# Optimization experiments

Measured on AMD Instinct MI355X. Metric: run time of the kernel, lower is better.

## Reference

```python
import jax, jax.numpy as jnp
import numpy as np

NUM_EXPERTS = 64
TOP_K = 8
N_GROUP = 8
TOPK_GROUP = 4
HIDDEN = 1024
INTER = 512
TOKENS = 2048


def setup_inputs() -> dict:
    key = jax.random.key(0)
    k1, k2, k3, k4 = jax.random.split(key, 4)
    return {
        "hidden_states": jax.random.normal(k1, (TOKENS, HIDDEN), jnp.float32),
        "gate_w": jax.random.normal(k2, (NUM_EXPERTS, HIDDEN), jnp.float32) * 0.02,
        "e_score_correction_bias": jnp.zeros((NUM_EXPERTS,), jnp.float32),
        "w13": jax.random.normal(k3, (NUM_EXPERTS, 2 * INTER, HIDDEN), jnp.float32) * 0.02,
        "w2": jax.random.normal(k4, (NUM_EXPERTS, HIDDEN, INTER), jnp.float32) * 0.02,
    }


def _grouped_topk(scores, bias):
    # DeepSeek-V3 style grouped top-k with sigmoid scores + correction bias.
    T, E = scores.shape
    s = scores + bias[None, :]                            # [T, E] selection scores
    sg = s.reshape(T, N_GROUP, E // N_GROUP)              # [T, G, E/G]
    top2 = jax.lax.top_k(sg, 2)[0]                        # [T, G, 2]
    group_scores = top2.sum(-1)                           # [T, G]
    _, gidx = jax.lax.top_k(group_scores, TOPK_GROUP)     # [T, topk_group]
    gmask = jnp.zeros((T, N_GROUP), bool).at[jnp.arange(T)[:, None], gidx].set(True)
    emask = jnp.repeat(gmask, E // N_GROUP, axis=1)       # [T, E]
    masked = jnp.where(emask, s, -jnp.inf)
    _, topk_ids = jax.lax.top_k(masked, TOP_K)            # [T, K]
    topk_w = jnp.take_along_axis(scores, topk_ids, axis=1)  # weights use raw scores (no bias)
    topk_w = topk_w / jnp.sum(topk_w, axis=-1, keepdims=True)  # renormalize (norm_topk_prob)
    return topk_w, topk_ids


def reference(hidden_states, gate_w, e_score_correction_bias, w13, w2):
    x = hidden_states                                      # [T, H]
    T, H = x.shape
    router_logits = x.astype(jnp.float32) @ gate_w.T       # fp32 gate, [T, E]
    scores = jax.nn.sigmoid(router_logits)
    topk_w, topk_ids = _grouped_topk(scores, e_score_correction_bias)
    # dense token->expert routing weights [T, E]
    R = jnp.zeros((T, NUM_EXPERTS), x.dtype).at[
        jnp.arange(T)[:, None], topk_ids
    ].add(topk_w.astype(x.dtype))

    def body(acc, inp):
        w13_e, w2_e, r_e = inp
        gu = x @ w13_e.T                                   # [T, 2I]
        g, u = jnp.split(gu, 2, axis=-1)
        h = jax.nn.silu(g) * u                             # SwiGLU
        return acc + r_e[:, None] * (h @ w2_e.T), None

    y, _ = jax.lax.scan(body, jnp.zeros_like(x), (w13, w2, R.T))
    return y
```

## Files before the change

### kernel.cpp

```cpp
#include <hip/hip_runtime.h>
#include <hip/hip_bf16.h>

#define TOKENS 2048
#define HDIM 1024
#define IDIM 512
#define NEXP 64
#define TOPKK 8
#define NGRP 8
#define TOPG 4

typedef __bf16 bf16_t;
typedef __bf16 bf16x8 __attribute__((ext_vector_type(8)));
typedef __bf16 bf16x4 __attribute__((ext_vector_type(4)));
typedef float f32x4 __attribute__((ext_vector_type(4)));

#define SWZ(r, b) ((b) ^ (((r) & 7) << 4))

__device__ inline bf16x8 pack_bf16x8(float4 a, float4 b) {
  bf16x8 r;
  r[0] = (bf16_t)a.x; r[1] = (bf16_t)a.y; r[2] = (bf16_t)a.z; r[3] = (bf16_t)a.w;
  r[4] = (bf16_t)b.x; r[5] = (bf16_t)b.y; r[6] = (bf16_t)b.z; r[7] = (bf16_t)b.w;
  return r;
}

__global__ __launch_bounds__(256) void cvt_x_kernel(const float* __restrict__ x,
                                                    bf16_t* __restrict__ xb) {
  int i = blockIdx.x * 256 + threadIdx.x;
  float4 v = reinterpret_cast<const float4*>(x)[i];
  bf16x4 o;
  o[0] = (bf16_t)v.x; o[1] = (bf16_t)v.y; o[2] = (bf16_t)v.z; o[3] = (bf16_t)v.w;
  reinterpret_cast<bf16x4*>(xb)[i] = o;
}

__global__ __launch_bounds__(256) void router_kernel(
    const float* __restrict__ x, const float* __restrict__ gw,
    const float* __restrict__ bias, int* __restrict__ counts,
    int* __restrict__ tok_list, int* __restrict__ dst_list,
    float* __restrict__ wgt_list) {
  int t0 = blockIdx.x * 16;
  int tid = threadIdx.x;
  int e = tid & 63;
  int sub = tid >> 6;

  const float4* gwe = reinterpret_cast<const float4*>(gw + (size_t)e * HDIM);
  const float4* x0 = reinterpret_cast<const float4*>(x + (size_t)(t0 + sub * 4 + 0) * HDIM);
  const float4* x1 = reinterpret_cast<const float4*>(x + (size_t)(t0 + sub * 4 + 1) * HDIM);
  const float4* x2 = reinterpret_cast<const float4*>(x + (size_t)(t0 + sub * 4 + 2) * HDIM);
  const float4* x3 = reinterpret_cast<const float4*>(x + (size_t)(t0 + sub * 4 + 3) * HDIM);
  float a0 = 0.f, a1 = 0.f, a2 = 0.f, a3 = 0.f;
  for (int h = 0; h < HDIM / 4; ++h) {
    float4 g = gwe[h];
    float4 v;
    v = x0[h]; a0 += g.x * v.x + g.y * v.y + g.z * v.z + g.w * v.w;
    v = x1[h]; a1 += g.x * v.x + g.y * v.y + g.z * v.z + g.w * v.w;
    v = x2[h]; a2 += g.x * v.x + g.y * v.y + g.z * v.z + g.w * v.w;
    v = x3[h]; a3 += g.x * v.x + g.y * v.y + g.z * v.z + g.w * v.w;
  }
  __shared__ float sc[16][64];
  sc[sub * 4 + 0][e] = a0;
  sc[sub * 4 + 1][e] = a1;
  sc[sub * 4 + 2][e] = a2;
  sc[sub * 4 + 3][e] = a3;
  __syncthreads();

  int lane = tid & 63;
  int wv = tid >> 6;
  for (int it = 0; it < 4; ++it) {
    int tt = wv * 4 + it;
    int t = t0 + tt;
    float logit = sc[tt][lane];
    float score = 1.0f / (1.0f + __expf(-logit));
    float s = score + bias[lane];

    float m1 = s, m2 = -INFINITY;
#pragma unroll
    for (int off = 1; off < 8; off <<= 1) {
      float o1 = __shfl_xor(m1, off);
      float o2 = __shfl_xor(m2, off);
      float hi = fmaxf(m1, o1);
      float lo = fminf(m1, o1);
      m2 = fmaxf(lo, fmaxf(m2, o2));
      m1 = hi;
    }
    float gscore = m1 + m2;
    int g = lane >> 3;
    int grank = 0;
#pragma unroll
    for (int gg = 0; gg < 8; ++gg) {
      float og = __shfl(gscore, gg << 3);
      grank += ((og > gscore) || (og == gscore && gg < g)) ? 1 : 0;
    }
    float masked = (grank < TOPG) ? s : -INFINITY;

    int rank = 0;
    for (int l = 0; l < 64; ++l) {
      float ov = __shfl(masked, l);
      rank += ((ov > masked) || (ov == masked && l < lane)) ? 1 : 0;
    }
    bool sel = (rank < TOPKK) && (masked > -INFINITY);
    float part = sel ? score : 0.0f;
#pragma unroll
    for (int off = 32; off > 0; off >>= 1) part += __shfl_xor(part, off);
    if (sel) {
      int slot = atomicAdd(&counts[lane], 1);
      tok_list[lane * TOKENS + slot] = t;
      dst_list[lane * TOKENS + slot] = t * TOPKK + rank;
      wgt_list[lane * TOKENS + slot] = score / part;
    }
  }
}

__global__ __launch_bounds__(256, 2) void gemm1_kernel(
    const bf16_t* __restrict__ xb, const float* __restrict__ w13,
    const int* __restrict__ counts, const int* __restrict__ tok_list,
    const int* __restrict__ dst_list, bf16_t* __restrict__ hbuf) {
  int e = blockIdx.z;
  int cnt = counts[e];
  int row0 = blockIdx.y * 256;
  if (row0 >= cnt) return;
  int rows = cnt - row0;
  if (rows > 256) rows = 256;
  int n0 = blockIdx.x * 64;

  __shared__ alignas(16) char As[256 * 128];
  __shared__ alignas(16) char Bg[64 * 128];
  __shared__ alignas(16) char Bu[64 * 128];
  __shared__ int dstS[256];

  int tid = threadIdx.x;
  int tok = -1;
  if (tid < rows) {
    tok = tok_list[e * TOKENS + row0 + tid];
    dstS[tid] = dst_list[e * TOKENS + row0 + tid];
  }
  const bf16_t* xrow = (tok >= 0) ? (xb + (size_t)tok * HDIM) : (const bf16_t*)0;

  int lane = tid & 63;
  int wv = tid >> 6;

  f32x4 accg[4][4], accu[4][4];
#pragma unroll
  for (int i = 0; i < 4; ++i)
#pragma unroll
    for (int j = 0; j < 4; ++j) {
      accg[i][j] = f32x4{0.f, 0.f, 0.f, 0.f};
      accu[i][j] = f32x4{0.f, 0.f, 0.f, 0.f};
    }

  const float* w13e = w13 + (size_t)e * (2 * IDIM) * HDIM;
  int bn = tid >> 2;
  int bq = tid & 3;
  const float* gsrc = w13e + (size_t)(n0 + bn) * HDIM + bq * 16;
  const float* usrc = w13e + (size_t)(IDIM + n0 + bn) * HDIM + bq * 16;

  for (int kt = 0; kt < 16; ++kt) {
    __syncthreads();
    if (tid < rows) {
      const bf16_t* src = xrow + kt * 64;
#pragma unroll
      for (int j = 0; j < 8; ++j) {
        bf16x8 v = *reinterpret_cast<const bf16x8*>(src + j * 8);
        *reinterpret_cast<bf16x8*>(&As[SWZ(tid, tid * 128 + j * 16)]) = v;
      }
    }
    {
      const float4* s4 = reinterpret_cast<const float4*>(gsrc + kt * 64);
      float4 f0 = s4[0], f1 = s4[1], f2 = s4[2], f3 = s4[3];
      int b0 = bn * 128 + bq * 32;
      *reinterpret_cast<bf16x8*>(&Bg[SWZ(bn, b0)]) = pack_bf16x8(f0, f1);
      *reinterpret_cast<bf16x8*>(&Bg[SWZ(bn, b0 + 16)]) = pack_bf16x8(f2, f3);
      const float4* u4 = reinterpret_cast<const float4*>(usrc + kt * 64);
      f0 = u4[0]; f1 = u4[1]; f2 = u4[2]; f3 = u4[3];
      *reinterpret_cast<bf16x8*>(&Bu[SWZ(bn, b0)]) = pack_bf16x8(f0, f1);
      *reinterpret_cast<bf16x8*>(&Bu[SWZ(bn, b0 + 16)]) = pack_bf16x8(f2, f3);
    }
    __syncthreads();
#pragma unroll
    for (int ks = 0; ks < 2; ++ks) {
      int kb2 = (ks * 32 + ((lane >> 4) << 3)) * 2;
      bf16x8 a[4], bg[4], bu[4];
#pragma unroll
      for (int i = 0; i < 4; ++i) {
        int r = wv * 64 + i * 16 + (lane & 15);
        a[i] = *reinterpret_cast<const bf16x8*>(&As[SWZ(r, r * 128 + kb2)]);
      }
#pragma unroll
      for (int j = 0; j < 4; ++j) {
        int n = j * 16 + (lane & 15);
        bg[j] = *reinterpret_cast<const bf16x8*>(&Bg[SWZ(n, n * 128 + kb2)]);
        bu[j] = *reinterpret_cast<const bf16x8*>(&Bu[SWZ(n, n * 128 + kb2)]);
      }
#pragma unroll
      for (int i = 0; i < 4; ++i)
#pragma unroll
        for (int j = 0; j < 4; ++j) {
          accg[i][j] = __builtin_amdgcn_mfma_f32_16x16x32_bf16(a[i], bg[j], accg[i][j], 0, 0, 0);
          accu[i][j] = __builtin_amdgcn_mfma_f32_16x16x32_bf16(a[i], bu[j], accu[i][j], 0, 0, 0);
        }
    }
  }
#pragma unroll
  for (int i = 0; i < 4; ++i) {
    int mbase = wv * 64 + i * 16 + ((lane >> 4) << 2);
#pragma unroll
    for (int r = 0; r < 4; ++r) {
      int m = mbase + r;
      if (m < rows) {
        int dst = dstS[m];
        bf16_t* hrow = hbuf + (size_t)dst * IDIM + n0;
#pragma unroll
        for (int j = 0; j < 4; ++j) {
          float gv = accg[i][j][r];
          float uv = accu[i][j][r];
          float hv = (gv / (1.0f + __expf(-gv))) * uv;
          hrow[j * 16 + (lane & 15)] = (bf16_t)hv;
        }
      }
    }
  }
}

__global__ __launch_bounds__(256, 2) void gemm2_kernel(
    const bf16_t* __restrict__ hbuf, const float* __restrict__ w2,
    const int* __restrict__ counts, const int* __restrict__ tok_list,
    const int* __restrict__ dst_list, const float* __restrict__ wgt_list,
    float* __restrict__ y) {
  int e = blockIdx.z;
  int cnt = counts[e];
  int row0 = blockIdx.y * 256;
  if (row0 >= cnt) return;
  int rows = cnt - row0;
  if (rows > 256) rows = 256;
  int n0 = blockIdx.x * 64;

  __shared__ alignas(16) char As[256 * 128];
  __shared__ alignas(16) char Bs[64 * 128];
  __shared__ int tokS[256];
  __shared__ float wS[256];

  int tid = threadIdx.x;
  int dst = -1;
  if (tid < rows) {
    tokS[tid] = tok_list[e * TOKENS + row0 + tid];
    dst = dst_list[e * TOKENS + row0 + tid];
    wS[tid] = wgt_list[e * TOKENS + row0 + tid];
  }
  const bf16_t* hrow = (dst >= 0) ? (hbuf + (size_t)dst * IDIM) : (const bf16_t*)0;

  int lane = tid & 63;
  int wv = tid >> 6;
  f32x4 acc[4][4];
#pragma unroll
  for (int i = 0; i < 4; ++i)
#pragma unroll
    for (int j = 0; j < 4; ++j) acc[i][j] = f32x4{0.f, 0.f, 0.f, 0.f};

  const float* w2e = w2 + (size_t)e * HDIM * IDIM;
  int bn = tid >> 2;
  int bq = tid & 3;
  const float* bsrc = w2e + (size_t)(n0 + bn) * IDIM + bq * 16;

  for (int kt = 0; kt < 8; ++kt) {
    __syncthreads();
    if (tid < rows) {
      const bf16_t* src = hrow + kt * 64;
#pragma unroll
      for (int j = 0; j < 8; ++j) {
        bf16x8 v = *reinterpret_cast<const bf16x8*>(src + j * 8);
        *reinterpret_cast<bf16x8*>(&As[SWZ(tid, tid * 128 + j * 16)]) = v;
      }
    }
    {
      const float4* s4 = reinterpret_cast<const float4*>(bsrc + kt * 64);
      float4 f0 = s4[0], f1 = s4[1], f2 = s4[2], f3 = s4[3];
      int b0 = bn * 128 + bq * 32;
      *reinterpret_cast<bf16x8*>(&Bs[SWZ(bn, b0)]) = pack_bf16x8(f0, f1);
      *reinterpret_cast<bf16x8*>(&Bs[SWZ(bn, b0 + 16)]) = pack_bf16x8(f2, f3);
    }
    __syncthreads();
#pragma unroll
    for (int ks = 0; ks < 2; ++ks) {
      int kb2 = (ks * 32 + ((lane >> 4) << 3)) * 2;
      bf16x8 a[4], b[4];
#pragma unroll
      for (int i = 0; i < 4; ++i) {
        int r = wv * 64 + i * 16 + (lane & 15);
        a[i] = *reinterpret_cast<const bf16x8*>(&As[SWZ(r, r * 128 + kb2)]);
      }
#pragma unroll
      for (int j = 0; j < 4; ++j) {
        int n = j * 16 + (lane & 15);
        b[j] = *reinterpret_cast<const bf16x8*>(&Bs[SWZ(n, n * 128 + kb2)]);
      }
#pragma unroll
      for (int i = 0; i < 4; ++i)
#pragma unroll
        for (int j = 0; j < 4; ++j)
          acc[i][j] = __builtin_amdgcn_mfma_f32_16x16x32_bf16(a[i], b[j], acc[i][j], 0, 0, 0);
    }
  }
#pragma unroll
  for (int i = 0; i < 4; ++i) {
    int mbase = wv * 64 + i * 16 + ((lane >> 4) << 2);
#pragma unroll
    for (int r = 0; r < 4; ++r) {
      int m = mbase + r;
      if (m < rows) {
        float wgt = wS[m];
        float* yrow = y + (size_t)tokS[m] * HDIM + n0;
#pragma unroll
        for (int j = 0; j < 4; ++j) {
          atomicAdd(&yrow[j * 16 + (lane & 15)], acc[i][j][r] * wgt);
        }
      }
    }
  }
}

extern "C" void kernel_launch(void* const* d_in, const int* in_sizes, int n_in,
                              void* d_out, int out_size, void* d_ws, size_t ws_size,
                              hipStream_t stream) {
  const float* x = (const float*)d_in[0];
  const float* gw = (const float*)d_in[1];
  const float* bias = (const float*)d_in[2];
  const float* w13 = (const float*)d_in[3];
  const float* w2 = (const float*)d_in[4];
  float* y = (float*)d_out;

  char* ws = (char*)d_ws;
  const size_t LIST = (size_t)NEXP * TOKENS * 4;
  int* counts = (int*)ws;
  int* tok_list = (int*)(ws + 1024);
  int* dst_list = (int*)(ws + 1024 + LIST);
  float* wgt_list = (float*)(ws + 1024 + 2 * LIST);
  bf16_t* xb = (bf16_t*)(ws + 1024 + 3 * LIST);
  bf16_t* hbuf = (bf16_t*)(ws + 1024 + 3 * LIST + (size_t)TOKENS * HDIM * 2);

  hipMemsetAsync(counts, 0, 1024, stream);
  hipMemsetAsync(y, 0, (size_t)TOKENS * HDIM * sizeof(float), stream);
  cvt_x_kernel<<<dim3(TOKENS * HDIM / 4 / 256), 256, 0, stream>>>(x, xb);
  router_kernel<<<dim3(TOKENS / 16), 256, 0, stream>>>(x, gw, bias, counts, tok_list,
                                                       dst_list, wgt_list);
  gemm1_kernel<<<dim3(IDIM / 64, 8, NEXP), 256, 0, stream>>>(xb, w13, counts, tok_list,
                                                             dst_list, hbuf);
  gemm2_kernel<<<dim3(HDIM / 64, 8, NEXP), 256, 0, stream>>>(hbuf, w2, counts, tok_list,
                                                             dst_list, wgt_list, y);
}
```

Before: 890.9 us.

## Prefetch next K-tile into registers during MFMA in both expert GEMM kernels

Both the gate/up and down-projection kernels now load the next K-slice of activations and fp32 weights into registers before running the MFMAs on the current slice, then write it to shared memory after a barrier. This register double-buffering is meant to hide global-memory latency behind the matrix math. A sched_barrier keeps the compiler from sinking the loads past the MFMAs. It costs extra registers, which can lower occupancy.

New measurement: 890.2 us. Within noise of the previous version (-0.1%).

```diff
diff --git a/kernel.cpp b/kernel.cpp
--- a/kernel.cpp
+++ b/kernel.cpp
@@ -152,29 +152,46 @@
   int bq = tid & 3;
   const float* gsrc = w13e + (size_t)(n0 + bn) * HDIM + bq * 16;
   const float* usrc = w13e + (size_t)(IDIM + n0 + bn) * HDIM + bq * 16;
+  int b0 = bn * 128 + bq * 32;
+
+  bf16x8 ra[8];
+  float4 rg[4], ru[4];
+
+  if (tid < rows) {
+#pragma unroll
+    for (int j = 0; j < 8; ++j) ra[j] = *reinterpret_cast<const bf16x8*>(xrow + j * 8);
+  }
+  {
+    const float4* g4 = reinterpret_cast<const float4*>(gsrc);
+    const float4* u4 = reinterpret_cast<const float4*>(usrc);
+#pragma unroll
+    for (int j = 0; j < 4; ++j) { rg[j] = g4[j]; ru[j] = u4[j]; }
+  }
+  if (tid < rows) {
+#pragma unroll
+    for (int j = 0; j < 8; ++j)
+      *reinterpret_cast<bf16x8*>(&As[SWZ(tid, tid * 128 + j * 16)]) = ra[j];
+  }
+  *reinterpret_cast<bf16x8*>(&Bg[SWZ(bn, b0)]) = pack_bf16x8(rg[0], rg[1]);
+  *reinterpret_cast<bf16x8*>(&Bg[SWZ(bn, b0 + 16)]) = pack_bf16x8(rg[2], rg[3]);
+  *reinterpret_cast<bf16x8*>(&Bu[SWZ(bn, b0)]) = pack_bf16x8(ru[0], ru[1]);
+  *reinterpret_cast<bf16x8*>(&Bu[SWZ(bn, b0 + 16)]) = pack_bf16x8(ru[2], ru[3]);
+  __syncthreads();
 
   for (int kt = 0; kt < 16; ++kt) {
-    __syncthreads();
-    if (tid < rows) {
-      const bf16_t* src = xrow + kt * 64;
-#pragma unroll
-      for (int j = 0; j < 8; ++j) {
-        bf16x8 v = *reinterpret_cast<const bf16x8*>(src + j * 8);
-        *reinterpret_cast<bf16x8*>(&As[SWZ(tid, tid * 128 + j * 16)]) = v;
-      }
-    }
-    {
-      const float4* s4 = reinterpret_cast<const float4*>(gsrc + kt * 64);
-      float4 f0 = s4[0], f1 = s4[1], f2 = s4[2], f3 = s4[3];
-      int b0 = bn * 128 + bq * 32;
-      *reinterpret_cast<bf16x8*>(&Bg[SWZ(bn, b0)]) = pack_bf16x8(f0, f1);
-      *reinterpret_cast<bf16x8*>(&Bg[SWZ(bn, b0 + 16)]) = pack_bf16x8(f2, f3);
-      const float4* u4 = reinterpret_cast<const float4*>(usrc + kt * 64);
-      f0 = u4[0]; f1 = u4[1]; f2 = u4[2]; f3 = u4[3];
-      *reinterpret_cast<bf16x8*>(&Bu[SWZ(bn, b0)]) = pack_bf16x8(f0, f1);
-      *reinterpret_cast<bf16x8*>(&Bu[SWZ(bn, b0 + 16)]) = pack_bf16x8(f2, f3);
-    }
-    __syncthreads();
+    if (kt < 15) {
+      if (tid < rows) {
+        const bf16_t* s = xrow + (kt + 1) * 64;
+#pragma unroll
+        for (int j = 0; j < 8; ++j) ra[j] = *reinterpret_cast<const bf16x8*>(s + j * 8);
+      }
+      const float4* g4 = reinterpret_cast<const float4*>(gsrc + (kt + 1) * 64);
+      const float4* u4 = reinterpret_cast<const float4*>(usrc + (kt + 1) * 64);
+#pragma unroll
+      for (int j = 0; j < 4; ++j) { rg[j] = g4[j]; ru[j] = u4[j]; }
+    }
+    __builtin_amdgcn_sched_barrier(0);
+
 #pragma unroll
     for (int ks = 0; ks < 2; ++ks) {
       int kb2 = (ks * 32 + ((lane >> 4) << 3)) * 2;
@@ -197,6 +214,19 @@
           accg[i][j] = __builtin_amdgcn_mfma_f32_16x16x32_bf16(a[i], bg[j], accg[i][j], 0, 0, 0);
           accu[i][j] = __builtin_amdgcn_mfma_f32_16x16x32_bf16(a[i], bu[j], accu[i][j], 0, 0, 0);
         }
+    }
+    __syncthreads();
+    if (kt < 15) {
+      if (tid < rows) {
+#pragma unroll
+        for (int j = 0; j < 8; ++j)
+          *reinterpret_cast<bf16x8*>(&As[SWZ(tid, tid * 128 + j * 16)]) = ra[j];
+      }
+      *reinterpret_cast<bf16x8*>(&Bg[SWZ(bn, b0)]) = pack_bf16x8(rg[0], rg[1]);
+      *reinterpret_cast<bf16x8*>(&Bg[SWZ(bn, b0 + 16)]) = pack_bf16x8(rg[2], rg[3]);
+      *reinterpret_cast<bf16x8*>(&Bu[SWZ(bn, b0)]) = pack_bf16x8(ru[0], ru[1]);
+      *reinterpret_cast<bf16x8*>(&Bu[SWZ(bn, b0 + 16)]) = pack_bf16x8(ru[2], ru[3]);
+      __syncthreads();
     }
   }
 #pragma unroll
@@ -259,25 +289,42 @@
   int bn = tid >> 2;
   int bq = tid & 3;
   const float* bsrc = w2e + (size_t)(n0 + bn) * IDIM + bq * 16;
+  int b0 = bn * 128 + bq * 32;
+
+  bf16x8 rh[8];
+  float4 rb[4];
+
+  if (tid < rows) {
+#pragma unroll
+    for (int j = 0; j < 8; ++j) rh[j] = *reinterpret_cast<const bf16x8*>(hrow + j * 8);
+  }
+  {
+    const float4* s4 = reinterpret_cast<const float4*>(bsrc);
+#pragma unroll
+    for (int j = 0; j < 4; ++j) rb[j] = s4[j];
+  }
+  if (tid < rows) {
+#pragma unroll
+    for (int j = 0; j < 8; ++j)
+      *reinterpret_cast<bf16x8*>(&As[SWZ(tid, tid * 128 + j * 16)]) = rh[j];
+  }
+  *reinterpret_cast<bf16x8*>(&Bs[SWZ(bn, b0)]) = pack_bf16x8(rb[0], rb[1]);
+  *reinterpret_cast<bf16x8*>(&Bs[SWZ(bn, b0 + 16)]) = pack_bf16x8(rb[2], rb[3]);
+  __syncthreads();
 
   for (int kt = 0; kt < 8; ++kt) {
-    __syncthreads();
-    if (tid < rows) {
-      const bf16_t* src = hrow + kt * 64;
-#pragma unroll
-      for (int j = 0; j < 8; ++j) {
-        bf16x8 v = *reinterpret_cast<const bf16x8*>(src + j * 8);
-        *reinterpret_cast<bf16x8*>(&As[SWZ(tid, tid * 128 + j * 16)]) = v;
-      }
-    }
-    {
-      const float4* s4 = reinterpret_cast<const float4*>(bsrc + kt * 64);
-      float4 f0 = s4[0], f1 = s4[1], f2 = s4[2], f3 = s4[3];
-      int b0 = bn * 128 + bq * 32;
-      *reinterpret_cast<bf16x8*>(&Bs[SWZ(bn, b0)]) = pack_bf16x8(f0, f1);
-      *reinterpret_cast<bf16x8*>(&Bs[SWZ(bn, b0 + 16)]) = pack_bf16x8(f2, f3);
-    }
-    __syncthreads();
+    if (kt < 7) {
+      if (tid < rows) {
+        const bf16_t* s = hrow + (kt + 1) * 64;
+#pragma unroll
+        for (int j = 0; j < 8; ++j) rh[j] = *reinterpret_cast<const bf16x8*>(s + j * 8);
+      }
+      const float4* s4 = reinterpret_cast<const float4*>(bsrc + (kt + 1) * 64);
+#pragma unroll
+      for (int j = 0; j < 4; ++j) rb[j] = s4[j];
+    }
+    __builtin_amdgcn_sched_barrier(0);
+
 #pragma unroll
     for (int ks = 0; ks < 2; ++ks) {
       int kb2 = (ks * 32 + ((lane >> 4) << 3)) * 2;
@@ -297,6 +344,17 @@
 #pragma unroll
         for (int j = 0; j < 4; ++j)
           acc[i][j] = __builtin_amdgcn_mfma_f32_16x16x32_bf16(a[i], b[j], acc[i][j], 0, 0, 0);
+    }
+    __syncthreads();
+    if (kt < 7) {
+      if (tid < rows) {
+#pragma unroll
+        for (int j = 0; j < 8; ++j)
+          *reinterpret_cast<bf16x8*>(&As[SWZ(tid, tid * 128 + j * 16)]) = rh[j];
+      }
+      *reinterpret_cast<bf16x8*>(&Bs[SWZ(bn, b0)]) = pack_bf16x8(rb[0], rb[1]);
+      *reinterpret_cast<bf16x8*>(&Bs[SWZ(bn, b0 + 16)]) = pack_bf16x8(rb[2], rb[3]);
+      __syncthreads();
     }
   }
 #pragma unroll
```
